# Optimization experiments

Hardware: AMD Instinct MI355X
Metric: run time of the kernel (lower is better)

## Reference

```python
import jax, jax.numpy as jnp
import numpy as np

IN_DIM, OUT_DIM, HID, L, PRED_LEN = 6, 6, 512, 4, 10


def _rnn_layer(x, Wih, Whh, bih, bhh):
    """Vanilla tanh RNN layer, batch_first x: [B,T,D] -> ([B,T,H], hT [B,H])."""
    B = x.shape[0]
    H = Whh.shape[0]
    xW = jnp.einsum('btd,hd->bth', x, Wih) + bih  # precompute input projections

    def step(h, xw_t):
        h = jnp.tanh(xw_t + h @ Whh.T + bhh)
        return h, h

    h0 = jnp.zeros((B, H), x.dtype)
    hT, ys = jax.lax.scan(step, h0, jnp.swapaxes(xW, 0, 1))
    return jnp.swapaxes(ys, 0, 1), hT


def setup_inputs() -> dict:
    key = jax.random.key(0)
    ks = jax.random.split(key, 16)
    s_in = 1.0 / np.sqrt(HID)
    u = lambda k, shp: jax.random.uniform(k, shp, jnp.float32, -s_in, s_in)
    inp = {
        'x': jax.random.normal(ks[0], (1024, 128, IN_DIM), jnp.float32),
        # encoder RNN params (layer 0 has input_dim=6, layers 1..3 have HID)
        'enc_Wih0': u(ks[1], (HID, IN_DIM)),
        'enc_Wih': u(ks[2], (L - 1, HID, HID)),
        'enc_Whh': u(ks[3], (L, HID, HID)),
        'enc_bih': u(ks[4], (L, HID)),
        'enc_bhh': u(ks[5], (L, HID)),
        # decoder RNN params (all layers take HID-dim input)
        'dec_Wih': u(ks[6], (L, HID, HID)),
        'dec_Whh': u(ks[7], (L, HID, HID)),
        'dec_bih': u(ks[8], (L, HID)),
        'dec_bhh': u(ks[9], (L, HID)),
        # output head
        'fc_W': u(ks[10], (OUT_DIM, HID)),
        'fc_b': u(ks[11], (OUT_DIM,)),
    }
    return inp


def reference(x, enc_Wih0, enc_Wih, enc_Whh, enc_bih, enc_bhh,
              dec_Wih, dec_Whh, dec_bih, dec_bhh, fc_W, fc_b):
    B = x.shape[0]
    # ---- encoder: 4-layer tanh RNN over src sequence ----
    h_enc = []
    out = x
    for l in range(L):
        Wih = enc_Wih0 if l == 0 else enc_Wih[l - 1]
        out, hT = _rnn_layer(out, Wih, enc_Whh[l], enc_bih[l], enc_bhh[l])
        h_enc.append(hT)
    enc_outputs = out                      # [B, T_src, HID]
    hidden = jnp.stack(h_enc)              # [L, B, HID]

    de_input0 = enc_outputs[:, -1, :]      # [B, HID]

    def dec_step(carry, _):
        inp, h = carry
        x_l = inp
        new_h = []
        for l in range(L):
            hl = jnp.tanh(x_l @ dec_Wih[l].T + dec_bih[l]
                          + h[l] @ dec_Whh[l].T + dec_bhh[l])
            new_h.append(hl)
            x_l = hl
        return (x_l, jnp.stack(new_h)), x_l

    _, ys = jax.lax.scan(dec_step, (de_input0, hidden), None, length=PRED_LEN)
    dec_out = jnp.swapaxes(ys, 0, 1)       # [B, PRED_LEN, HID]
    outputs = dec_out @ fc_W.T + fc_b      # [B, PRED_LEN, OUT_DIM]
    return enc_outputs, outputs
```

## Files before the change

### kernel.cpp

```cpp
#include <hip/hip_runtime.h>

typedef _Float16 f16;
typedef _Float16 f16x8 __attribute__((ext_vector_type(8)));
typedef float    f32x4 __attribute__((ext_vector_type(4)));
typedef unsigned long long u64;

#define TSEQ 128
#define PRED 10

__global__ void k_cvt(const float* __restrict__ src, f16* __restrict__ dst, int n) {
  int i = blockIdx.x * blockDim.x + threadIdx.x;
  int stride = gridDim.x * blockDim.x;
  for (; i < n; i += stride) dst[i] = (f16)src[i];
}

__global__ void k_bias(const float* __restrict__ a, const float* __restrict__ b,
                       float* __restrict__ o, int n) {
  int i = blockIdx.x * blockDim.x + threadIdx.x;
  if (i < n) o[i] = a[i] + b[i];
}

__global__ __launch_bounds__(256) void k_gemm_xw(
    const f16* __restrict__ A, const f16* __restrict__ W,
    const float* __restrict__ bias, f16* __restrict__ C) {
  __shared__ f16 As[128 * 72];
  __shared__ f16 Bs[256 * 72];
  const int tid = threadIdx.x;
  const int w = tid >> 6, lane = tid & 63;
  const int wm = w >> 1, wn = w & 1;
  const int q = lane >> 4, l15 = lane & 15;
  const int m0 = blockIdx.x * 128;
  const int n0 = blockIdx.y * 256;

  f32x4 acc[4][8];
  const f32x4 zero = {0.f, 0.f, 0.f, 0.f};
#pragma unroll
  for (int i = 0; i < 4; i++)
#pragma unroll
    for (int j = 0; j < 8; j++) acc[i][j] = zero;

  for (int k0 = 0; k0 < 512; k0 += 64) {
    __syncthreads();
#pragma unroll
    for (int i = 0; i < 4; i++) {
      int ch = tid + 256 * i; int r = ch >> 3, kc = ch & 7;
      *(f16x8*)&As[r * 72 + kc * 8] = *(const f16x8*)&A[(size_t)(m0 + r) * 512 + k0 + kc * 8];
    }
#pragma unroll
    for (int i = 0; i < 8; i++) {
      int ch = tid + 256 * i; int r = ch >> 3, kc = ch & 7;
      *(f16x8*)&Bs[r * 72 + kc * 8] = *(const f16x8*)&W[(size_t)(n0 + r) * 512 + k0 + kc * 8];
    }
    __syncthreads();
#pragma unroll
    for (int kk = 0; kk < 2; kk++) {
      f16x8 af[4], bf[8];
#pragma unroll
      for (int mt = 0; mt < 4; mt++)
        af[mt] = *(const f16x8*)&As[(wm * 64 + mt * 16 + l15) * 72 + kk * 32 + q * 8];
#pragma unroll
      for (int nt = 0; nt < 8; nt++)
        bf[nt] = *(const f16x8*)&Bs[(wn * 128 + nt * 16 + l15) * 72 + kk * 32 + q * 8];
#pragma unroll
      for (int mt = 0; mt < 4; mt++)
#pragma unroll
        for (int nt = 0; nt < 8; nt++)
          acc[mt][nt] = __builtin_amdgcn_mfma_f32_16x16x32_f16(af[mt], bf[nt], acc[mt][nt], 0, 0, 0);
    }
  }
#pragma unroll
  for (int mt = 0; mt < 4; mt++)
#pragma unroll
    for (int nt = 0; nt < 8; nt++)
#pragma unroll
      for (int r = 0; r < 4; r++) {
        int mg = m0 + wm * 64 + mt * 16 + q * 4 + r;
        int ng = n0 + wn * 128 + nt * 16 + l15;
        C[(size_t)mg * 512 + ng] = (f16)(acc[mt][nt][r] + bias[ng]);
      }
}

__global__ __launch_bounds__(256) void k_enc_rec(
    const f16* __restrict__ xw, const float* __restrict__ x,
    const float* __restrict__ Wih0, const float* __restrict__ bias0,
    const f16* __restrict__ Whh, f16* __restrict__ out_h,
    float* __restrict__ out_f, f16* __restrict__ hT,
    f16* __restrict__ hx, int* __restrict__ ctr, int is_l0) {
  __shared__ f16 As[16 * 520];
  __shared__ float xs[16][8];
  const int tid = threadIdx.x;
  const int w = tid >> 6, lane = tid & 63, q = lane >> 4, l15 = lane & 15;
  const int c = blockIdx.x & 63, sub = blockIdx.x >> 6;
  const int row0 = c * 16;
  const int ncol0 = sub * 128 + w * 32;
  int* myctr = ctr + c * 32;

  f16x8 Bfr[2][16];
#pragma unroll
  for (int t2 = 0; t2 < 2; t2++) {
    int ng = ncol0 + t2 * 16 + l15;
#pragma unroll
    for (int kk = 0; kk < 16; kk++)
      Bfr[t2][kk] = *(const f16x8*)&Whh[(size_t)ng * 512 + kk * 32 + q * 8];
  }

  float w0[2][6]; float b0[2];
  if (is_l0) {
#pragma unroll
    for (int t2 = 0; t2 < 2; t2++) {
      int ng = ncol0 + t2 * 16 + l15;
#pragma unroll
      for (int d = 0; d < 6; d++) w0[t2][d] = Wih0[ng * 6 + d];
      b0[t2] = bias0[ng];
    }
  }

  for (int i = tid; i < 16 * 520; i += 256) As[i] = (f16)0.0f;
  if (is_l0 && tid < 96) xs[tid / 6][tid % 6] = x[(size_t)(row0 + tid / 6) * TSEQ * 6 + tid % 6];
  __syncthreads();

  for (int t = 0; t < TSEQ; t++) {
    const int p = t & 1;
    f16 xwr[2][4];
    if (!is_l0) {
#pragma unroll
      for (int t2 = 0; t2 < 2; t2++)
#pragma unroll
        for (int r = 0; r < 4; r++)
          xwr[t2][r] = xw[((size_t)(row0 + q * 4 + r) * TSEQ + t) * 512 + ncol0 + t2 * 16 + l15];
    }

    const f32x4 zero = {0.f, 0.f, 0.f, 0.f};
    f32x4 acc0 = zero, acc1 = zero;
#pragma unroll
    for (int kk = 0; kk < 16; kk++) {
      f16x8 a = *(const f16x8*)&As[l15 * 520 + kk * 32 + q * 8];
      acc0 = __builtin_amdgcn_mfma_f32_16x16x32_f16(a, Bfr[0][kk], acc0, 0, 0, 0);
      acc1 = __builtin_amdgcn_mfma_f32_16x16x32_f16(a, Bfr[1][kk], acc1, 0, 0, 0);
    }

    float hv[2][4];
    union { u64 u; f16 h4[4]; } pk[2];
#pragma unroll
    for (int t2 = 0; t2 < 2; t2++) {
      f32x4 accv = t2 ? acc1 : acc0;
#pragma unroll
      for (int r = 0; r < 4; r++) {
        int m = q * 4 + r;
        float pre;
        if (is_l0) {
          float xwv = b0[t2];
#pragma unroll
          for (int d = 0; d < 6; d++) xwv += xs[m][d] * w0[t2][d];
          pre = accv[r] + xwv;
        } else {
          pre = accv[r] + (float)xwr[t2][r];
        }
        hv[t2][r] = tanhf(pre);
        pk[t2].h4[r] = (f16)hv[t2][r];
      }
    }

    if (t < TSEQ - 1) {
#pragma unroll
      for (int t2 = 0; t2 < 2; t2++) {
        int ng = ncol0 + t2 * 16 + l15;
        __hip_atomic_store(
            (u64*)&hx[(((size_t)p * 64 + c) * 512 + ng) * 16 + q * 4],
            pk[t2].u, __ATOMIC_RELAXED, __HIP_MEMORY_SCOPE_AGENT);
      }
      __builtin_amdgcn_s_waitcnt(0);
      __syncthreads();
      if (tid == 0)
        __hip_atomic_fetch_add(myctr, 1, __ATOMIC_RELAXED, __HIP_MEMORY_SCOPE_AGENT);
    }

#pragma unroll
    for (int t2 = 0; t2 < 2; t2++) {
      int ng = ncol0 + t2 * 16 + l15;
#pragma unroll
      for (int r = 0; r < 4; r++) {
        int b = row0 + q * 4 + r;
        out_h[((size_t)b * TSEQ + t) * 512 + ng] = pk[t2].h4[r];
        if (out_f) out_f[((size_t)b * TSEQ + t) * 512 + ng] = hv[t2][r];
        if (t == TSEQ - 1) hT[(size_t)b * 512 + ng] = pk[t2].h4[r];
      }
    }
    if (t == TSEQ - 1) break;

    if (tid == 0) {
      int target = 4 * (t + 1);
      while (__hip_atomic_load(myctr, __ATOMIC_RELAXED, __HIP_MEMORY_SCOPE_AGENT) < target)
        __builtin_amdgcn_s_sleep(1);
    }
    __syncthreads();

    {
      u64 v[8];
#pragma unroll
      for (int cc = 0; cc < 2; cc++) {
        int col = tid * 2 + cc;
        const u64* bp = (const u64*)&hx[(((size_t)p * 64 + c) * 512 + col) * 16];
#pragma unroll
        for (int j = 0; j < 4; j++)
          v[cc * 4 + j] = __hip_atomic_load(bp + j, __ATOMIC_RELAXED, __HIP_MEMORY_SCOPE_AGENT);
      }
      union { u64 u[4]; f16 h[16]; } un0, un1;
      un0.u[0] = v[0]; un0.u[1] = v[1]; un0.u[2] = v[2]; un0.u[3] = v[3];
      un1.u[0] = v[4]; un1.u[1] = v[5]; un1.u[2] = v[6]; un1.u[3] = v[7];
#pragma unroll
      for (int k = 0; k < 16; k++) {
        union { f16 h2[2]; unsigned int u; } pw;
        pw.h2[0] = un0.h[k]; pw.h2[1] = un1.h[k];
        *(unsigned int*)&As[k * 520 + tid * 2] = pw.u;
      }
    }
    if (is_l0 && tid < 96)
      xs[tid / 6][tid % 6] = x[((size_t)(row0 + tid / 6) * TSEQ + (t + 1)) * 6 + tid % 6];
    __syncthreads();
  }
}

__global__ __launch_bounds__(256) void k_dec_rec(
    const f16* __restrict__ Wih, const f16* __restrict__ Whh,
    const float* __restrict__ decB, const f16* __restrict__ hT,
    f16* __restrict__ hstate, f16* __restrict__ dec_out, int* __restrict__ ctr) {
  __shared__ f16 xb[16 * 520];
  __shared__ f16 hb[16 * 520];
  const int tid = threadIdx.x;
  const int w = tid >> 6, lane = tid & 63, q = lane >> 4, l15 = lane & 15;
  const int c = blockIdx.x >> 2, sub = blockIdx.x & 3;
  const int row0 = c * 16;
  const int ncol0 = sub * 128 + w * 32;
  int* myctr = ctr + c * 32;
  const size_t LSZ = (size_t)1024 * 512;

  auto load_rm = [&](f16* dst, const f16* src) {
#pragma unroll
    for (int i = 0; i < 4; i++) {
      int idx = tid + 256 * i; int m = idx >> 6, kc = idx & 63;
      *(f16x8*)&dst[m * 520 + kc * 8] = *(const f16x8*)&src[(size_t)(row0 + m) * 512 + kc * 8];
    }
  };
  auto load_cm = [&](f16* dst, int buf) {
    u64 v[8];
#pragma unroll
    for (int cc = 0; cc < 2; cc++) {
      int col = tid * 2 + cc;
      const u64* bp = (const u64*)&hstate[(((size_t)buf * 64 + c) * 512 + col) * 16];
#pragma unroll
      for (int j = 0; j < 4; j++)
        v[cc * 4 + j] = __hip_atomic_load(bp + j, __ATOMIC_RELAXED, __HIP_MEMORY_SCOPE_AGENT);
    }
    union { u64 u[4]; f16 h[16]; } un0, un1;
    un0.u[0] = v[0]; un0.u[1] = v[1]; un0.u[2] = v[2]; un0.u[3] = v[3];
    un1.u[0] = v[4]; un1.u[1] = v[5]; un1.u[2] = v[6]; un1.u[3] = v[7];
#pragma unroll
    for (int k = 0; k < 16; k++) {
      union { f16 h2[2]; unsigned int u; } pw;
      pw.h2[0] = un0.h[k]; pw.h2[1] = un1.h[k];
      *(unsigned int*)&dst[k * 520 + tid * 2] = pw.u;
    }
  };

  for (int s = 0; s < PRED; s++) {
    int wb = (s + 1) & 1, rb = s & 1;
    for (int l = 0; l < 4; l++) {
      const bool last = (s == PRED - 1) && (l == 3);
      if (l == 0) {
        if (s == 0) load_rm(xb, hT + 3 * LSZ);
        else load_cm(xb, rb * 4 + 3);
      } else {
        load_cm(xb, wb * 4 + (l - 1));
      }
      if (s == 0) load_rm(hb, hT + (size_t)l * LSZ);
      else load_cm(hb, rb * 4 + l);
      __syncthreads();

      const f32x4 zero = {0.f, 0.f, 0.f, 0.f};
      f32x4 acc0 = zero, acc1 = zero;
      const f16* Wl = Wih + (size_t)l * 512 * 512;
      const f16* Ul = Whh + (size_t)l * 512 * 512;
      int ng0 = ncol0 + l15, ng1 = ncol0 + 16 + l15;
#pragma unroll
      for (int kk = 0; kk < 16; kk++) {
        f16x8 a = *(const f16x8*)&xb[l15 * 520 + kk * 32 + q * 8];
        f16x8 bv0 = *(const f16x8*)&Wl[(size_t)ng0 * 512 + kk * 32 + q * 8];
        f16x8 bv1 = *(const f16x8*)&Wl[(size_t)ng1 * 512 + kk * 32 + q * 8];
        acc0 = __builtin_amdgcn_mfma_f32_16x16x32_f16(a, bv0, acc0, 0, 0, 0);
        acc1 = __builtin_amdgcn_mfma_f32_16x16x32_f16(a, bv1, acc1, 0, 0, 0);
      }
#pragma unroll
      for (int kk = 0; kk < 16; kk++) {
        f16x8 a = *(const f16x8*)&hb[l15 * 520 + kk * 32 + q * 8];
        f16x8 bv0 = *(const f16x8*)&Ul[(size_t)ng0 * 512 + kk * 32 + q * 8];
        f16x8 bv1 = *(const f16x8*)&Ul[(size_t)ng1 * 512 + kk * 32 + q * 8];
        acc0 = __builtin_amdgcn_mfma_f32_16x16x32_f16(a, bv0, acc0, 0, 0, 0);
        acc1 = __builtin_amdgcn_mfma_f32_16x16x32_f16(a, bv1, acc1, 0, 0, 0);
      }

      int obuf = wb * 4 + l;
      union { u64 u; f16 h4[4]; } pk[2];
#pragma unroll
      for (int t2 = 0; t2 < 2; t2++) {
        f32x4 accv = t2 ? acc1 : acc0;
        int ng = ncol0 + t2 * 16 + l15;
#pragma unroll
        for (int r = 0; r < 4; r++)
          pk[t2].h4[r] = (f16)tanhf(accv[r] + decB[l * 512 + ng]);
      }

      if (!last) {
#pragma unroll
        for (int t2 = 0; t2 < 2; t2++) {
          int ng = ncol0 + t2 * 16 + l15;
          __hip_atomic_store(
              (u64*)&hstate[(((size_t)obuf * 64 + c) * 512 + ng) * 16 + q * 4],
              pk[t2].u, __ATOMIC_RELAXED, __HIP_MEMORY_SCOPE_AGENT);
        }
        __builtin_amdgcn_s_waitcnt(0);
        __syncthreads();
        if (tid == 0)
          __hip_atomic_fetch_add(myctr, 1, __ATOMIC_RELAXED, __HIP_MEMORY_SCOPE_AGENT);
      }

      if (l == 3) {
#pragma unroll
        for (int t2 = 0; t2 < 2; t2++) {
          int ng = ncol0 + t2 * 16 + l15;
#pragma unroll
          for (int r = 0; r < 4; r++)
            dec_out[((size_t)(row0 + q * 4 + r) * PRED + s) * 512 + ng] = pk[t2].h4[r];
        }
      }

      if (!last) {
        if (tid == 0) {
          int target = 4 * (s * 4 + l + 1);
          while (__hip_atomic_load(myctr, __ATOMIC_RELAXED, __HIP_MEMORY_SCOPE_AGENT) < target)
            __builtin_amdgcn_s_sleep(1);
        }
        __syncthreads();
      }
    }
  }
}

__global__ __launch_bounds__(256) void k_fc(
    const f16* __restrict__ dec_out, const float* __restrict__ fcW,
    const float* __restrict__ fcb, float* __restrict__ out) {
  __shared__ float Wl[6 * 512];
  __shared__ float bl[8];
  int tid = threadIdx.x;
  for (int i = tid; i < 3072; i += 256) Wl[i] = fcW[i];
  if (tid < 6) bl[tid] = fcb[tid];
  __syncthreads();
  int g = blockIdx.x * 256 + tid;
  const f16* row = dec_out + (size_t)g * 512;
  float acc[6] = {0, 0, 0, 0, 0, 0};
  for (int kc = 0; kc < 64; kc++) {
    f16x8 xv = *(const f16x8*)&row[kc * 8];
#pragma unroll
    for (int j = 0; j < 8; j++) {
      float xf = (float)xv[j];
#pragma unroll
      for (int o = 0; o < 6; o++) acc[o] += xf * Wl[o * 512 + kc * 8 + j];
    }
  }
#pragma unroll
  for (int o = 0; o < 6; o++) out[(size_t)g * 6 + o] = acc[o] + bl[o];
}

extern "C" void kernel_launch(void* const* d_in, const int* in_sizes, int n_in,
                              void* d_out, int out_size, void* d_ws, size_t ws_size,
                              hipStream_t stream) {
  const float* x      = (const float*)d_in[0];
  const float* Wih0   = (const float*)d_in[1];
  const float* eWih32 = (const float*)d_in[2];
  const float* eWhh32 = (const float*)d_in[3];
  const float* ebih   = (const float*)d_in[4];
  const float* ebhh   = (const float*)d_in[5];
  const float* dWih32 = (const float*)d_in[6];
  const float* dWhh32 = (const float*)d_in[7];
  const float* dbih   = (const float*)d_in[8];
  const float* dbhh   = (const float*)d_in[9];
  const float* fcW    = (const float*)d_in[10];
  const float* fcb    = (const float*)d_in[11];
  float* outp = (float*)d_out;

  char* ws = (char*)d_ws;
  size_t off = 0;
  auto alloc = [&](size_t bytes) { void* p = ws + off; off += (bytes + 255) & ~255ULL; return p; };
  f16* outA   = (f16*)alloc((size_t)131072 * 512 * 2);
  f16* xwB    = (f16*)alloc((size_t)131072 * 512 * 2);
  f16* eWih   = (f16*)alloc((size_t)3 * 262144 * 2);
  f16* eWhh   = (f16*)alloc((size_t)4 * 262144 * 2);
  f16* dWih   = (f16*)alloc((size_t)4 * 262144 * 2);
  f16* dWhh   = (f16*)alloc((size_t)4 * 262144 * 2);
  float* encB = (float*)alloc(2048 * 4);
  float* decB = (float*)alloc(2048 * 4);
  f16* hT     = (f16*)alloc((size_t)4 * 1024 * 512 * 2);
  f16* hstate = (f16*)alloc((size_t)8 * 1024 * 512 * 2);
  f16* hx     = (f16*)alloc((size_t)2 * 1024 * 512 * 2);
  f16* dec_o  = (f16*)alloc((size_t)1024 * 10 * 512 * 2);
  int* ctr    = (int*)alloc(5 * 64 * 32 * 4);

  hipMemsetAsync(ctr, 0, 5 * 64 * 32 * 4, stream);
  k_cvt<<<512, 256, 0, stream>>>(eWih32, eWih, 3 * 262144);
  k_cvt<<<512, 256, 0, stream>>>(eWhh32, eWhh, 4 * 262144);
  k_cvt<<<512, 256, 0, stream>>>(dWih32, dWih, 4 * 262144);
  k_cvt<<<512, 256, 0, stream>>>(dWhh32, dWhh, 4 * 262144);
  k_bias<<<8, 256, 0, stream>>>(ebih, ebhh, encB, 2048);
  k_bias<<<8, 256, 0, stream>>>(dbih, dbhh, decB, 2048);

  k_enc_rec<<<256, 256, 0, stream>>>(nullptr, x, Wih0, encB, eWhh, outA, nullptr, hT, hx, ctr, 1);
  for (int l = 1; l < 4; l++) {
    k_gemm_xw<<<dim3(1024, 2), 256, 0, stream>>>(outA, eWih + (size_t)(l - 1) * 262144,
                                                 encB + l * 512, xwB);
    float* of = (l == 3) ? outp : nullptr;
    k_enc_rec<<<256, 256, 0, stream>>>(xwB, nullptr, nullptr, nullptr,
                                       eWhh + (size_t)l * 262144, outA, of,
                                       hT + (size_t)l * 524288, hx, ctr + l * 2048, 0);
  }
  k_dec_rec<<<256, 256, 0, stream>>>(dWih, dWhh, decB, hT, hstate, dec_o, ctr + 4 * 2048);
  k_fc<<<40, 256, 0, stream>>>(dec_o, fcW, fcb, outp + (size_t)1024 * 128 * 512);
}
```

Measured before the change: 3.151 ms.

## Fuse all four encoder layers into one wavefront-pipelined persistent kernel

Replaces the per-layer sequence (input-projection GEMM plus recurrent kernel, four times) with a single persistent kernel of 512 blocks. Each block owns one layer, a 32-row batch chunk and a column slice, so the layers run as a wavefront across time. Each layer reads the layer below's hidden state at step t from a 4-deep ring buffer, using producer/consumer counters for flow control, and computes the input projection inline with MFMA. This removes the large intermediate xW and outA buffers and the serialization between layers. In exchange, weights are read from global/L2 every step instead of being held in registers, and the cross-block spin-waits depend on all 512 blocks being co-resident.

```diff
diff --git a/kernel.cpp b/kernel.cpp
--- a/kernel.cpp
+++ b/kernel.cpp
@@ -20,204 +20,202 @@
   if (i < n) o[i] = a[i] + b[i];
 }
 
-__global__ __launch_bounds__(256) void k_gemm_xw(
-    const f16* __restrict__ A, const f16* __restrict__ W,
-    const float* __restrict__ bias, f16* __restrict__ C) {
-  __shared__ f16 As[128 * 72];
-  __shared__ f16 Bs[256 * 72];
-  const int tid = threadIdx.x;
-  const int w = tid >> 6, lane = tid & 63;
-  const int wm = w >> 1, wn = w & 1;
-  const int q = lane >> 4, l15 = lane & 15;
-  const int m0 = blockIdx.x * 128;
-  const int n0 = blockIdx.y * 256;
-
-  f32x4 acc[4][8];
-  const f32x4 zero = {0.f, 0.f, 0.f, 0.f};
-#pragma unroll
-  for (int i = 0; i < 4; i++)
-#pragma unroll
-    for (int j = 0; j < 8; j++) acc[i][j] = zero;
-
-  for (int k0 = 0; k0 < 512; k0 += 64) {
-    __syncthreads();
-#pragma unroll
-    for (int i = 0; i < 4; i++) {
-      int ch = tid + 256 * i; int r = ch >> 3, kc = ch & 7;
-      *(f16x8*)&As[r * 72 + kc * 8] = *(const f16x8*)&A[(size_t)(m0 + r) * 512 + k0 + kc * 8];
-    }
-#pragma unroll
-    for (int i = 0; i < 8; i++) {
-      int ch = tid + 256 * i; int r = ch >> 3, kc = ch & 7;
-      *(f16x8*)&Bs[r * 72 + kc * 8] = *(const f16x8*)&W[(size_t)(n0 + r) * 512 + k0 + kc * 8];
-    }
-    __syncthreads();
-#pragma unroll
-    for (int kk = 0; kk < 2; kk++) {
-      f16x8 af[4], bf[8];
-#pragma unroll
-      for (int mt = 0; mt < 4; mt++)
-        af[mt] = *(const f16x8*)&As[(wm * 64 + mt * 16 + l15) * 72 + kk * 32 + q * 8];
-#pragma unroll
-      for (int nt = 0; nt < 8; nt++)
-        bf[nt] = *(const f16x8*)&Bs[(wn * 128 + nt * 16 + l15) * 72 + kk * 32 + q * 8];
-#pragma unroll
-      for (int mt = 0; mt < 4; mt++)
-#pragma unroll
-        for (int nt = 0; nt < 8; nt++)
-          acc[mt][nt] = __builtin_amdgcn_mfma_f32_16x16x32_f16(af[mt], bf[nt], acc[mt][nt], 0, 0, 0);
-    }
-  }
-#pragma unroll
-  for (int mt = 0; mt < 4; mt++)
-#pragma unroll
-    for (int nt = 0; nt < 8; nt++)
-#pragma unroll
-      for (int r = 0; r < 4; r++) {
-        int mg = m0 + wm * 64 + mt * 16 + q * 4 + r;
-        int ng = n0 + wn * 128 + nt * 16 + l15;
-        C[(size_t)mg * 512 + ng] = (f16)(acc[mt][nt][r] + bias[ng]);
-      }
-}
-
-__global__ __launch_bounds__(256) void k_enc_rec(
-    const f16* __restrict__ xw, const float* __restrict__ x,
-    const float* __restrict__ Wih0, const float* __restrict__ bias0,
-    const f16* __restrict__ Whh, f16* __restrict__ out_h,
-    float* __restrict__ out_f, f16* __restrict__ hT,
-    f16* __restrict__ hx, int* __restrict__ ctr, int is_l0) {
-  __shared__ f16 As[16 * 520];
-  __shared__ float xs[16][8];
+__global__ __launch_bounds__(256) void k_enc_wave(
+    const float* __restrict__ x, const float* __restrict__ Wih0,
+    const f16* __restrict__ eWih, const float* __restrict__ encB,
+    const f16* __restrict__ eWhh, float* __restrict__ out_f,
+    f16* __restrict__ hT, u64* __restrict__ hx,
+    int* __restrict__ ctr, int* __restrict__ cons) {
+  __shared__ f16 As[32 * 520];
+  __shared__ float xs[32][8];
   const int tid = threadIdx.x;
   const int w = tid >> 6, lane = tid & 63, q = lane >> 4, l15 = lane & 15;
-  const int c = blockIdx.x & 63, sub = blockIdx.x >> 6;
-  const int row0 = c * 16;
-  const int ncol0 = sub * 128 + w * 32;
-  int* myctr = ctr + c * 32;
-
-  f16x8 Bfr[2][16];
-#pragma unroll
-  for (int t2 = 0; t2 < 2; t2++) {
-    int ng = ncol0 + t2 * 16 + l15;
-#pragma unroll
-    for (int kk = 0; kk < 16; kk++)
-      Bfr[t2][kk] = *(const f16x8*)&Whh[(size_t)ng * 512 + kk * 32 + q * 8];
+  const int bid = blockIdx.x;
+  const int layer = bid & 3, sub = (bid >> 2) & 3, c = bid >> 4;
+  const int row0 = c * 32, ncol0 = sub * 128 + w * 32;
+  const int is_l0 = (layer == 0), is_top = (layer == 3);
+  int* myctr = ctr + (layer * 32 + c) * 32;
+  int* upctr = is_l0 ? nullptr : ctr + ((layer - 1) * 32 + c) * 32;
+  int* mycons = is_l0 ? nullptr : cons + ((layer - 1) * 32 + c) * 32;
+  int* pcons  = is_top ? nullptr : cons + (layer * 32 + c) * 32;
+  const f16* Whh = eWhh + (size_t)layer * 262144;
+  const f16* Wt  = is_l0 ? (const f16*)nullptr : eWih + (size_t)(layer - 1) * 262144;
+  u64* HXmy = hx + (size_t)layer * 524288;
+  u64* HXup = is_l0 ? nullptr : hx + (size_t)(layer - 1) * 524288;
+  f16* myhT = hT + (size_t)layer * 524288;
+
+  float w0[2][6], b0[2], tb[2];
+  if (is_l0) {
+#pragma unroll
+    for (int ct = 0; ct < 2; ct++) {
+      int ng = ncol0 + ct * 16 + l15;
+#pragma unroll
+      for (int d = 0; d < 6; d++) w0[ct][d] = Wih0[ng * 6 + d];
+      b0[ct] = encB[ng];
+    }
+  } else {
+    tb[0] = encB[layer * 512 + ncol0 + l15];
+    tb[1] = encB[layer * 512 + ncol0 + 16 + l15];
   }
 
-  float w0[2][6]; float b0[2];
-  if (is_l0) {
-#pragma unroll
-    for (int t2 = 0; t2 < 2; t2++) {
-      int ng = ncol0 + t2 * 16 + l15;
-#pragma unroll
-      for (int d = 0; d < 6; d++) w0[t2][d] = Wih0[ng * 6 + d];
-      b0[t2] = bias0[ng];
-    }
-  }
-
-  for (int i = tid; i < 16 * 520; i += 256) As[i] = (f16)0.0f;
-  if (is_l0 && tid < 96) xs[tid / 6][tid % 6] = x[(size_t)(row0 + tid / 6) * TSEQ * 6 + tid % 6];
+  for (int i = tid; i < 32 * 520; i += 256) As[i] = (f16)0.0f;
+  if (is_l0 && tid < 192)
+    xs[tid / 6][tid % 6] = x[((size_t)(row0 + tid / 6) * TSEQ + 0) * 6 + tid % 6];
   __syncthreads();
 
+  const int k0 = tid * 2;
+
   for (int t = 0; t < TSEQ; t++) {
-    const int p = t & 1;
-    f16 xwr[2][4];
+    int pcv = 0x7fffffff;
+    if (pcons && t >= 4)
+      pcv = __hip_atomic_load(pcons, __ATOMIC_RELAXED, __HIP_MEMORY_SCOPE_AGENT);
+
+    if (tid == 0) {
+      if (t > 0)
+        while (__hip_atomic_load(myctr, __ATOMIC_RELAXED, __HIP_MEMORY_SCOPE_AGENT) < 4 * t)
+          __builtin_amdgcn_s_sleep(1);
+      if (!is_l0)
+        while (__hip_atomic_load(upctr, __ATOMIC_RELAXED, __HIP_MEMORY_SCOPE_AGENT) < 4 * (t + 1))
+          __builtin_amdgcn_s_sleep(1);
+    }
+    __syncthreads();
+
+    u64 uv[16];
     if (!is_l0) {
-#pragma unroll
-      for (int t2 = 0; t2 < 2; t2++)
-#pragma unroll
-        for (int r = 0; r < 4; r++)
-          xwr[t2][r] = xw[((size_t)(row0 + q * 4 + r) * TSEQ + t) * 512 + ncol0 + t2 * 16 + l15];
-    }
+      const u64* ub = HXup + ((size_t)(t & 3) * 32 + c) * 4096 + (size_t)k0 * 8;
+#pragma unroll
+      for (int j = 0; j < 16; j++)
+        uv[j] = __hip_atomic_load(ub + j, __ATOMIC_RELAXED, __HIP_MEMORY_SCOPE_AGENT);
+    }
+    if (t > 0) {
+      u64 ov[16];
+      const u64* ob = HXmy + ((size_t)((t - 1) & 3) * 32 + c) * 4096 + (size_t)k0 * 8;
+#pragma unroll
+      for (int j = 0; j < 16; j++)
+        ov[j] = __hip_atomic_load(ob + j, __ATOMIC_RELAXED, __HIP_MEMORY_SCOPE_AGENT);
+      union U { u64 u[8]; f16 h[32]; } u0, u1;
+#pragma unroll
+      for (int j = 0; j < 8; j++) { u0.u[j] = ov[j]; u1.u[j] = ov[8 + j]; }
+#pragma unroll
+      for (int row = 0; row < 32; row++) {
+        union { f16 h2[2]; unsigned int wv; } pw;
+        pw.h2[0] = u0.h[row]; pw.h2[1] = u1.h[row];
+        *(unsigned int*)&As[row * 520 + k0] = pw.wv;
+      }
+      if (is_l0 && tid < 192)
+        xs[tid / 6][tid % 6] = x[((size_t)(row0 + tid / 6) * TSEQ + t) * 6 + tid % 6];
+    }
+    __syncthreads();
 
     const f32x4 zero = {0.f, 0.f, 0.f, 0.f};
-    f32x4 acc0 = zero, acc1 = zero;
-#pragma unroll
-    for (int kk = 0; kk < 16; kk++) {
-      f16x8 a = *(const f16x8*)&As[l15 * 520 + kk * 32 + q * 8];
-      acc0 = __builtin_amdgcn_mfma_f32_16x16x32_f16(a, Bfr[0][kk], acc0, 0, 0, 0);
-      acc1 = __builtin_amdgcn_mfma_f32_16x16x32_f16(a, Bfr[1][kk], acc1, 0, 0, 0);
-    }
-
-    float hv[2][4];
-    union { u64 u; f16 h4[4]; } pk[2];
-#pragma unroll
-    for (int t2 = 0; t2 < 2; t2++) {
-      f32x4 accv = t2 ? acc1 : acc0;
-#pragma unroll
-      for (int r = 0; r < 4; r++) {
-        int m = q * 4 + r;
-        float pre;
-        if (is_l0) {
-          float xwv = b0[t2];
-#pragma unroll
-          for (int d = 0; d < 6; d++) xwv += xs[m][d] * w0[t2][d];
-          pre = accv[r] + xwv;
-        } else {
-          pre = accv[r] + (float)xwr[t2][r];
+    f32x4 acc[2][2] = {{zero, zero}, {zero, zero}};
+    {
+      const f16* bp0 = &Whh[(size_t)(ncol0 + l15) * 512 + q * 8];
+      const f16* bp1 = &Whh[(size_t)(ncol0 + 16 + l15) * 512 + q * 8];
+#pragma unroll
+      for (int kk = 0; kk < 16; kk++) {
+        f16x8 a0 = *(const f16x8*)&As[l15 * 520 + kk * 32 + q * 8];
+        f16x8 a1 = *(const f16x8*)&As[(16 + l15) * 520 + kk * 32 + q * 8];
+        f16x8 b0v = *(const f16x8*)(bp0 + kk * 32);
+        f16x8 b1v = *(const f16x8*)(bp1 + kk * 32);
+        acc[0][0] = __builtin_amdgcn_mfma_f32_16x16x32_f16(a0, b0v, acc[0][0], 0, 0, 0);
+        acc[0][1] = __builtin_amdgcn_mfma_f32_16x16x32_f16(a0, b1v, acc[0][1], 0, 0, 0);
+        acc[1][0] = __builtin_amdgcn_mfma_f32_16x16x32_f16(a1, b0v, acc[1][0], 0, 0, 0);
+        acc[1][1] = __builtin_amdgcn_mfma_f32_16x16x32_f16(a1, b1v, acc[1][1], 0, 0, 0);
+      }
+    }
+
+    if (!is_l0) {
+      __syncthreads();
+      union U { u64 u[8]; f16 h[32]; } u0, u1;
+#pragma unroll
+      for (int j = 0; j < 8; j++) { u0.u[j] = uv[j]; u1.u[j] = uv[8 + j]; }
+#pragma unroll
+      for (int row = 0; row < 32; row++) {
+        union { f16 h2[2]; unsigned int wv; } pw;
+        pw.h2[0] = u0.h[row]; pw.h2[1] = u1.h[row];
+        *(unsigned int*)&As[row * 520 + k0] = pw.wv;
+      }
+      __syncthreads();
+      const f16* wp0 = &Wt[(size_t)(ncol0 + l15) * 512 + q * 8];
+      const f16* wp1 = &Wt[(size_t)(ncol0 + 16 + l15) * 512 + q * 8];
+#pragma unroll
+      for (int kk = 0; kk < 16; kk++) {
+        f16x8 a0 = *(const f16x8*)&As[l15 * 520 + kk * 32 + q * 8];
+        f16x8 a1 = *(const f16x8*)&As[(16 + l15) * 520 + kk * 32 + q * 8];
+        f16x8 b0v = *(const f16x8*)(wp0 + kk * 32);
+        f16x8 b1v = *(const f16x8*)(wp1 + kk * 32);
+        acc[0][0] = __builtin_amdgcn_mfma_f32_16x16x32_f16(a0, b0v, acc[0][0], 0, 0, 0);
+        acc[0][1] = __builtin_amdgcn_mfma_f32_16x16x32_f16(a0, b1v, acc[0][1], 0, 0, 0);
+        acc[1][0] = __builtin_amdgcn_mfma_f32_16x16x32_f16(a1, b0v, acc[1][0], 0, 0, 0);
+        acc[1][1] = __builtin_amdgcn_mfma_f32_16x16x32_f16(a1, b1v, acc[1][1], 0, 0, 0);
+      }
+    }
+
+    float hv[2][2][4];
+    union { u64 u; f16 h4[4]; } pk[2][2];
+#pragma unroll
+    for (int ct = 0; ct < 2; ct++)
+#pragma unroll
+      for (int mt = 0; mt < 2; mt++)
+#pragma unroll
+        for (int r = 0; r < 4; r++) {
+          int m = mt * 16 + q * 4 + r;
+          float pre;
+          if (is_l0) {
+            float xwv = b0[ct];
+#pragma unroll
+            for (int d = 0; d < 6; d++) xwv += xs[m][d] * w0[ct][d];
+            pre = acc[mt][ct][r] + xwv;
+          } else {
+            pre = acc[mt][ct][r] + tb[ct];
+          }
+          hv[ct][mt][r] = tanhf(pre);
+          pk[ct][mt].h4[r] = (f16)hv[ct][mt][r];
         }
-        hv[t2][r] = tanhf(pre);
-        pk[t2].h4[r] = (f16)hv[t2][r];
-      }
-    }
-
-    if (t < TSEQ - 1) {
-#pragma unroll
-      for (int t2 = 0; t2 < 2; t2++) {
-        int ng = ncol0 + t2 * 16 + l15;
-        __hip_atomic_store(
-            (u64*)&hx[(((size_t)p * 64 + c) * 512 + ng) * 16 + q * 4],
-            pk[t2].u, __ATOMIC_RELAXED, __HIP_MEMORY_SCOPE_AGENT);
-      }
-      __builtin_amdgcn_s_waitcnt(0);
-      __syncthreads();
-      if (tid == 0)
-        __hip_atomic_fetch_add(myctr, 1, __ATOMIC_RELAXED, __HIP_MEMORY_SCOPE_AGENT);
-    }
-
-#pragma unroll
-    for (int t2 = 0; t2 < 2; t2++) {
-      int ng = ncol0 + t2 * 16 + l15;
-#pragma unroll
-      for (int r = 0; r < 4; r++) {
-        int b = row0 + q * 4 + r;
-        out_h[((size_t)b * TSEQ + t) * 512 + ng] = pk[t2].h4[r];
-        if (out_f) out_f[((size_t)b * TSEQ + t) * 512 + ng] = hv[t2][r];
-        if (t == TSEQ - 1) hT[(size_t)b * 512 + ng] = pk[t2].h4[r];
-      }
-    }
-    if (t == TSEQ - 1) break;
-
+
+    if (pcons && t >= 4 && pcv < 4 * (t - 3)) {
+      while (__hip_atomic_load(pcons, __ATOMIC_RELAXED, __HIP_MEMORY_SCOPE_AGENT) < 4 * (t - 3))
+        __builtin_amdgcn_s_sleep(1);
+    }
+
+    {
+      u64* pb = HXmy + ((size_t)(t & 3) * 32 + c) * 4096;
+#pragma unroll
+      for (int ct = 0; ct < 2; ct++)
+#pragma unroll
+        for (int mt = 0; mt < 2; mt++)
+          __hip_atomic_store(pb + (size_t)(ncol0 + ct * 16 + l15) * 8 + mt * 4 + q,
+                             pk[ct][mt].u, __ATOMIC_RELAXED, __HIP_MEMORY_SCOPE_AGENT);
+    }
+    __builtin_amdgcn_s_waitcnt(0);
+    __syncthreads();
     if (tid == 0) {
-      int target = 4 * (t + 1);
-      while (__hip_atomic_load(myctr, __ATOMIC_RELAXED, __HIP_MEMORY_SCOPE_AGENT) < target)
-        __builtin_amdgcn_s_sleep(1);
-    }
-    __syncthreads();
-
-    {
-      u64 v[8];
-#pragma unroll
-      for (int cc = 0; cc < 2; cc++) {
-        int col = tid * 2 + cc;
-        const u64* bp = (const u64*)&hx[(((size_t)p * 64 + c) * 512 + col) * 16];
-#pragma unroll
-        for (int j = 0; j < 4; j++)
-          v[cc * 4 + j] = __hip_atomic_load(bp + j, __ATOMIC_RELAXED, __HIP_MEMORY_SCOPE_AGENT);
-      }
-      union { u64 u[4]; f16 h[16]; } un0, un1;
-      un0.u[0] = v[0]; un0.u[1] = v[1]; un0.u[2] = v[2]; un0.u[3] = v[3];
-      un1.u[0] = v[4]; un1.u[1] = v[5]; un1.u[2] = v[6]; un1.u[3] = v[7];
-#pragma unroll
-      for (int k = 0; k < 16; k++) {
-        union { f16 h2[2]; unsigned int u; } pw;
-        pw.h2[0] = un0.h[k]; pw.h2[1] = un1.h[k];
-        *(unsigned int*)&As[k * 520 + tid * 2] = pw.u;
-      }
-    }
-    if (is_l0 && tid < 96)
-      xs[tid / 6][tid % 6] = x[((size_t)(row0 + tid / 6) * TSEQ + (t + 1)) * 6 + tid % 6];
-    __syncthreads();
+      __hip_atomic_fetch_add(myctr, 1, __ATOMIC_RELAXED, __HIP_MEMORY_SCOPE_AGENT);
+      if (!is_l0)
+        __hip_atomic_fetch_add(mycons, 1, __ATOMIC_RELAXED, __HIP_MEMORY_SCOPE_AGENT);
+    }
+
+    if (is_top) {
+#pragma unroll
+      for (int ct = 0; ct < 2; ct++)
+#pragma unroll
+        for (int mt = 0; mt < 2; mt++)
+#pragma unroll
+          for (int r = 0; r < 4; r++)
+            out_f[((size_t)(row0 + mt * 16 + q * 4 + r) * TSEQ + t) * 512 +
+                  (ncol0 + ct * 16 + l15)] = hv[ct][mt][r];
+    }
+    if (t == TSEQ - 1) {
+#pragma unroll
+      for (int ct = 0; ct < 2; ct++)
+#pragma unroll
+        for (int mt = 0; mt < 2; mt++)
+#pragma unroll
+          for (int r = 0; r < 4; r++)
+            myhT[(size_t)(row0 + mt * 16 + q * 4 + r) * 512 + ncol0 + ct * 16 + l15] =
+                pk[ct][mt].h4[r];
+    }
   }
 }
 
@@ -391,8 +389,6 @@
   char* ws = (char*)d_ws;
   size_t off = 0;
   auto alloc = [&](size_t bytes) { void* p = ws + off; off += (bytes + 255) & ~255ULL; return p; };
-  f16* outA   = (f16*)alloc((size_t)131072 * 512 * 2);
-  f16* xwB    = (f16*)alloc((size_t)131072 * 512 * 2);
   f16* eWih   = (f16*)alloc((size_t)3 * 262144 * 2);
   f16* eWhh   = (f16*)alloc((size_t)4 * 262144 * 2);
   f16* dWih   = (f16*)alloc((size_t)4 * 262144 * 2);
@@ -401,11 +397,15 @@
   float* decB = (float*)alloc(2048 * 4);
   f16* hT     = (f16*)alloc((size_t)4 * 1024 * 512 * 2);
   f16* hstate = (f16*)alloc((size_t)8 * 1024 * 512 * 2);
-  f16* hx     = (f16*)alloc((size_t)2 * 1024 * 512 * 2);
+  u64* hx     = (u64*)alloc((size_t)4 * 524288 * 8);
   f16* dec_o  = (f16*)alloc((size_t)1024 * 10 * 512 * 2);
-  int* ctr    = (int*)alloc(5 * 64 * 32 * 4);
-
-  hipMemsetAsync(ctr, 0, 5 * 64 * 32 * 4, stream);
+  int* ctrE   = (int*)alloc(4 * 32 * 32 * 4);
+  int* consA  = (int*)alloc(3 * 32 * 32 * 4);
+  int* ctrD   = (int*)alloc(64 * 32 * 4);
+
+  size_t syncsz = (char*)(ctrD + 64 * 32) - (char*)ctrE;
+  hipMemsetAsync(ctrE, 0, syncsz, stream);
+
   k_cvt<<<512, 256, 0, stream>>>(eWih32, eWih, 3 * 262144);
   k_cvt<<<512, 256, 0, stream>>>(eWhh32, eWhh, 4 * 262144);
   k_cvt<<<512, 256, 0, stream>>>(dWih32, dWih, 4 * 262144);
@@ -413,15 +413,8 @@
   k_bias<<<8, 256, 0, stream>>>(ebih, ebhh, encB, 2048);
   k_bias<<<8, 256, 0, stream>>>(dbih, dbhh, decB, 2048);
 
-  k_enc_rec<<<256, 256, 0, stream>>>(nullptr, x, Wih0, encB, eWhh, outA, nullptr, hT, hx, ctr, 1);
-  for (int l = 1; l < 4; l++) {
-    k_gemm_xw<<<dim3(1024, 2), 256, 0, stream>>>(outA, eWih + (size_t)(l - 1) * 262144,
-                                                 encB + l * 512, xwB);
-    float* of = (l == 3) ? outp : nullptr;
-    k_enc_rec<<<256, 256, 0, stream>>>(xwB, nullptr, nullptr, nullptr,
-                                       eWhh + (size_t)l * 262144, outA, of,
-                                       hT + (size_t)l * 524288, hx, ctr + l * 2048, 0);
-  }
-  k_dec_rec<<<256, 256, 0, stream>>>(dWih, dWhh, decB, hT, hstate, dec_o, ctr + 4 * 2048);
+  k_enc_wave<<<512, 256, 0, stream>>>(x, Wih0, eWih, encB, eWhh, outp, hT, hx,
+                                      ctrE, consA);
+  k_dec_rec<<<256, 256, 0, stream>>>(dWih, dWhh, decB, hT, hstate, dec_o, ctrD);
   k_fc<<<40, 256, 0, stream>>>(dec_o, fcW, fcb, outp + (size_t)1024 * 128 * 512);
 }
```

Measured after the change: 4.605 ms. 46.2% more time.
